# Kernel optimization log

Hardware: AMD Instinct MI355X
Metric: run time of the kernel (lower is better)

The kernel has to match this reference:

```python
import jax, jax.numpy as jnp
import numpy as np

NUM_NODES = 50000
NUM_OBSERVED = 512
BATCH = 2048


def setup_inputs() -> dict:
    key = jax.random.key(0)
    inputs = jax.random.normal(key, (BATCH, NUM_OBSERVED), dtype=jnp.float32)
    # 512 unique, strided node ids in [0, NUM_NODES): 511*97 = 49567 < 50000
    node_indices = (jnp.arange(NUM_OBSERVED, dtype=jnp.int64) * 97)
    return {"inputs": inputs, "node_indices": node_indices}


def reference(inputs, node_indices):
    # Faithful to: full = inputs @ one_hot(node_indices, NUM_NODES); full[..., None]
    # One-hot matmul sums contributions at duplicate indices, so scatter-ADD
    # (not set) reproduces the exact math without the dense [K, N] GEMM.
    batch = inputs.shape[0]
    full = jnp.zeros((batch, NUM_NODES), dtype=inputs.dtype)
    full = full.at[:, node_indices].add(inputs)  # [B, N]
    return full[..., None]  # [B, N, 1]
```

## Files before the change

kernel.cpp:

```cpp
#include <hip/hip_runtime.h>


__global__ void init_map_kernel(int* __restrict__ map, int n) {
    int i = blockIdx.x * blockDim.x + threadIdx.x;
    if (i < n) map[i] = -1;
}

__global__ void fill_map_kernel(const int* __restrict__ idx, int k,
                                int* __restrict__ map) {
    int j = blockIdx.x * blockDim.x + threadIdx.x;
    if (j < k) map[idx[j]] = j;
}

__global__ __launch_bounds__(256) void fused_scatter_kernel(
    const float* __restrict__ in,
    const int*   __restrict__ map,
    float*       __restrict__ out,
    int K, int n4)
{
    int g = blockIdx.x * blockDim.x + threadIdx.x;
    if (g >= n4) return;
    int b = blockIdx.y;

    const int4 m = ((const int4*)map)[g];
    const float* row = in + (size_t)b * K;

    float4 v = make_float4(0.f, 0.f, 0.f, 0.f);
    if (m.x >= 0) v.x = row[m.x];
    if (m.y >= 0) v.y = row[m.y];
    if (m.z >= 0) v.z = row[m.z];
    if (m.w >= 0) v.w = row[m.w];

    ((float4*)out)[(size_t)b * n4 + g] = v;
}

extern "C" void kernel_launch(void* const* d_in, const int* in_sizes, int n_in,
                              void* d_out, int out_size, void* d_ws, size_t ws_size,
                              hipStream_t stream) {
    const float* in  = (const float*)d_in[0];
    const int*   idx = (const int*)d_in[1];
    float*       out = (float*)d_out;

    const int K = in_sizes[1];
    const int B = in_sizes[0] / K;
    const int N = out_size / B;
    const int n4 = N / 4;

    int* map = (int*)d_ws;

    init_map_kernel<<<(N + 255) / 256, 256, 0, stream>>>(map, N);
    fill_map_kernel<<<(K + 255) / 256, 256, 0, stream>>>(idx, K, map);

    dim3 grid((n4 + 255) / 256, B);
    fused_scatter_kernel<<<grid, 256, 0, stream>>>(in, map, out, K, n4);
}
```

Measured before the change: 443.8 us.

## Flatten scatter into grid-stride loop with nontemporal vector stores

Replaces the 2D grid (column blocks × batch rows) with a fixed 2048-block grid-stride loop over the flattened batch×column float4 space, tracking row and column incrementally. Output writes become nontemporal stores so the roughly 400 MB zero-dominated output stream does not pollute caches. The persistent loop trades fewer blocks for per-iteration index arithmetic and may lower memory-level parallelism if too few waves stay resident.

```diff
diff --git a/kernel.cpp b/kernel.cpp
--- a/kernel.cpp
+++ b/kernel.cpp
@@ -1,5 +1,11 @@
 #include <hip/hip_runtime.h>
 
+
+#define TPB 256
+#define BLOCKS 2048
+
+typedef float v4f __attribute__((ext_vector_type(4)));
+typedef int   v4i __attribute__((ext_vector_type(4)));
 
 __global__ void init_map_kernel(int* __restrict__ map, int n) {
     int i = blockIdx.x * blockDim.x + threadIdx.x;
@@ -12,26 +18,37 @@
     if (j < k) map[idx[j]] = j;
 }
 
-__global__ __launch_bounds__(256) void fused_scatter_kernel(
+__global__ __launch_bounds__(TPB) void fused_flat_kernel(
     const float* __restrict__ in,
     const int*   __restrict__ map,
     float*       __restrict__ out,
-    int K, int n4)
+    int K, int n4, unsigned total4)
 {
-    int g = blockIdx.x * blockDim.x + threadIdx.x;
-    if (g >= n4) return;
-    int b = blockIdx.y;
+    const unsigned stride = gridDim.x * TPB;
+    unsigned g = blockIdx.x * TPB + threadIdx.x;
+    if (g >= total4) return;
 
-    const int4 m = ((const int4*)map)[g];
-    const float* row = in + (size_t)b * K;
+    unsigned b = g / (unsigned)n4;
+    unsigned c = g - b * (unsigned)n4;
+    const unsigned sdiv = stride / (unsigned)n4;
+    const unsigned smod = stride - sdiv * (unsigned)n4;
 
-    float4 v = make_float4(0.f, 0.f, 0.f, 0.f);
-    if (m.x >= 0) v.x = row[m.x];
-    if (m.y >= 0) v.y = row[m.y];
-    if (m.z >= 0) v.z = row[m.z];
-    if (m.w >= 0) v.w = row[m.w];
+    const v4i* map4 = (const v4i*)map;
+    v4f*       out4 = (v4f*)out;
 
-    ((float4*)out)[(size_t)b * n4 + g] = v;
+    for (; g < total4; g += stride) {
+        const v4i m = map4[c];
+        const float* row = in + (size_t)b * K;
+        v4f v = (v4f)(0.f);
+        if (m.x >= 0) v.x = row[m.x];
+        if (m.y >= 0) v.y = row[m.y];
+        if (m.z >= 0) v.z = row[m.z];
+        if (m.w >= 0) v.w = row[m.w];
+        __builtin_nontemporal_store(v, out4 + g);
+
+        b += sdiv; c += smod;
+        if (c >= (unsigned)n4) { c -= (unsigned)n4; ++b; }
+    }
 }
 
 extern "C" void kernel_launch(void* const* d_in, const int* in_sizes, int n_in,
@@ -45,12 +62,12 @@
     const int B = in_sizes[0] / K;
     const int N = out_size / B;
     const int n4 = N / 4;
+    const unsigned total4 = (unsigned)B * (unsigned)n4;
 
     int* map = (int*)d_ws;
 
     init_map_kernel<<<(N + 255) / 256, 256, 0, stream>>>(map, N);
     fill_map_kernel<<<(K + 255) / 256, 256, 0, stream>>>(idx, K, map);
 
-    dim3 grid((n4 + 255) / 256, B);
-    fused_scatter_kernel<<<grid, 256, 0, stream>>>(in, map, out, K, n4);
+    fused_flat_kernel<<<BLOCKS, TPB, 0, stream>>>(in, map, out, K, n4, total4);
 }
```

Result: faster. 430.7 us (-2.9%).
